# Performance work log

Measured on AMD Instinct MI355X. Metric: run time of the kernel, lower is better.

The kernel has to match this reference:

```python
import jax, jax.numpy as jnp
import numpy as np

MAX_DISPARITY = 48  # disparity range [0, 48] -> 49 hypotheses


def setup_inputs() -> dict:
    key = jax.random.key(0)
    k1, k2, k3, k4 = jax.random.split(key, 4)
    B, C, H, W = 1, 64, 256, 512
    C_out = 16
    return {
        "left_embedding": jax.random.normal(k1, (B, C, H, W), dtype=jnp.float32),
        "right_embedding": jax.random.normal(k2, (B, C, H, W), dtype=jnp.float32),
        "W_op": jax.random.normal(k3, (C_out, 2 * C), dtype=jnp.float32) * 0.05,
        "b_op": jax.random.normal(k4, (C_out,), dtype=jnp.float32) * 0.05,
    }


def reference(left_embedding, right_embedding, W_op, b_op):
    # operation(cat([L, R_shift], dim=1)) with a 1x1 conv is linear, so it
    # splits into W_l @ L + W_r @ R_shift; shifting commutes with the 1x1 conv,
    # so we apply the conv ONCE to each embedding and shift the small result.
    D = MAX_DISPARITY
    B, C, H, W = left_embedding.shape
    W_l, W_r = W_op[:, :C], W_op[:, C:]
    L = jnp.einsum('oc,bcyx->boyx', W_l, left_embedding)    # [B,O,H,W]
    R = jnp.einsum('oc,bcyx->boyx', W_r, right_embedding)   # [B,O,H,W]
    # ZeroPad2d((D, 0, 0, 0)): pad D zeros on the LEFT of the x axis
    R_pad = jnp.pad(R, ((0, 0), (0, 0), (0, 0), (D, 0)))
    # disparity d reads padded[..., D-d : D-d+W] -> idx[d, x] = D - d + x
    idx = (D - jnp.arange(D + 1))[:, None] + jnp.arange(W)[None, :]  # [D+1, W]
    R_shift = R_pad[:, :, :, idx]                  # [B,O,H,D+1,W]
    R_shift = jnp.transpose(R_shift, (0, 1, 3, 2, 4))  # [B,O,D+1,H,W]
    out = L[:, :, None, :, :] + R_shift + b_op[None, :, None, None, None]
    return out  # [batch, feature, disparity, y, x]
```

## Files before the change

kernel.cpp:

```cpp
#include <hip/hip_runtime.h>

#define HH 256
#define WW 512
#define CC 64
#define CO 16
#define DD 48
#define ND (DD + 1)

typedef float f32x4 __attribute__((ext_vector_type(4)));

__global__ __launch_bounds__(256) void lr_project(
    const float* __restrict__ left, const float* __restrict__ right,
    const float* __restrict__ Wop, const float* __restrict__ bop,
    float* __restrict__ Lout, float* __restrict__ Rout)
{
    const int tid = blockIdx.x * blockDim.x + threadIdx.x;
    const int x = tid & (WW - 1);
    const int y = tid >> 9;

    float accL[CO], accR[CO];
#pragma unroll
    for (int o = 0; o < CO; ++o) { accL[o] = 0.0f; accR[o] = 0.0f; }

#pragma unroll 4
    for (int c = 0; c < CC; ++c) {
        const float l = left [(c * HH + y) * WW + x];
        const float r = right[(c * HH + y) * WW + x];
#pragma unroll
        for (int o = 0; o < CO; ++o) {
            accL[o] += Wop[o * (2 * CC) + c]      * l;
            accR[o] += Wop[o * (2 * CC) + CC + c] * r;
        }
    }

#pragma unroll
    for (int o = 0; o < CO; ++o) {
        Lout[(o * HH + y) * WW + x] = accL[o] + bop[o];
        Rout[(o * HH + y) * WW + x] = accR[o];
    }
}

__global__ __launch_bounds__(256) void assemble_plane(
    const float* __restrict__ L, const float* __restrict__ R,
    float* __restrict__ out)
{
    const int g = blockIdx.x & 7;
    const int j = blockIdx.x >> 3;
    const int o = 2 * g + (j / ND);
    const int d = j % ND;
    const int od = o * ND + d;

    const int t  = threadIdx.x;
    const int x4 = t & 127;
    const int y0 = t >> 7;
    const int x  = x4 * 4;

    const float m0 = (x + 0 >= d) ? 1.0f : 0.0f;
    const float m1 = (x + 1 >= d) ? 1.0f : 0.0f;
    const float m2 = (x + 2 >= d) ? 1.0f : 0.0f;
    const float m3 = (x + 3 >= d) ? 1.0f : 0.0f;

    const float* Lp = &L[(o * HH + y0) * WW + x];
    const float* Rp = Lp + (R - L) - d;
    float*       op = &out[((size_t)od * HH + y0) * WW + x];

#pragma unroll 4
    for (int k = 0; k < HH / 2; ++k) {
        const f32x4 lv = *reinterpret_cast<const f32x4*>(Lp);
        f32x4 rv;
        __builtin_memcpy(&rv, Rp, sizeof(rv));

        f32x4 ov;
        ov.x = lv.x + m0 * rv.x;
        ov.y = lv.y + m1 * rv.y;
        ov.z = lv.z + m2 * rv.z;
        ov.w = lv.w + m3 * rv.w;
        __builtin_nontemporal_store(ov, reinterpret_cast<f32x4*>(op));

        Lp += 2 * WW;
        Rp += 2 * WW;
        op += 2 * WW;
    }
}

extern "C" void kernel_launch(void* const* d_in, const int* in_sizes, int n_in,
                              void* d_out, int out_size, void* d_ws, size_t ws_size,
                              hipStream_t stream) {
    const float* left  = (const float*)d_in[0];
    const float* right = (const float*)d_in[1];
    const float* Wop   = (const float*)d_in[2];
    const float* bop   = (const float*)d_in[3];
    float* out = (float*)d_out;

    float* Lws = (float*)d_ws;
    float* Rws = Lws + (size_t)CO * HH * WW;

    lr_project<<<(HH * WW) / 256, 256, 0, stream>>>(left, right, Wop, bop, Lws, Rws);

    assemble_plane<<<CO * ND, 256, 0, stream>>>(Lws, Rws, out);
}
```

Baseline: 123.9 us.

## Replace per-plane assembly with persistent wave-linear streaming over output

The broadcast-add kernel becomes a fixed grid of 1024 waves, each streaming a contiguous 392×1KB span of the output. It splits the span at (feature, disparity) plane boundaries to recompute the shift and masks. Odd half-rows skip the mask multiply, since only x<48 can need masking. Stores switch from nontemporal to normal cached stores. Work is split evenly across waves with long sequential write runs, at the cost of per-segment bookkeeping and possible cache pollution from the regular stores.

```diff
diff --git a/kernel.cpp b/kernel.cpp
--- a/kernel.cpp
+++ b/kernel.cpp
@@ -40,46 +40,58 @@
     }
 }
 
-__global__ __launch_bounds__(256) void assemble_plane(
+__global__ __launch_bounds__(256) void assemble_stream(
     const float* __restrict__ L, const float* __restrict__ R,
     float* __restrict__ out)
 {
-    const int g = blockIdx.x & 7;
-    const int j = blockIdx.x >> 3;
-    const int o = 2 * g + (j / ND);
-    const int d = j % ND;
-    const int od = o * ND + d;
+    const int tid  = blockIdx.x * blockDim.x + threadIdx.x;
+    const int wave = tid >> 6;
+    const int lane = tid & 63;
 
-    const int t  = threadIdx.x;
-    const int x4 = t & 127;
-    const int y0 = t >> 7;
-    const int x  = x4 * 4;
+    int v = wave * 392;
+    const int vend = v + 392;
 
-    const float m0 = (x + 0 >= d) ? 1.0f : 0.0f;
-    const float m1 = (x + 1 >= d) ? 1.0f : 0.0f;
-    const float m2 = (x + 2 >= d) ? 1.0f : 0.0f;
-    const float m3 = (x + 3 >= d) ? 1.0f : 0.0f;
+    float* op = out + (size_t)v * 256 + lane * 4;
+    const ptrdiff_t RminusL = R - L;
 
-    const float* Lp = &L[(o * HH + y0) * WW + x];
-    const float* Rp = Lp + (R - L) - d;
-    float*       op = &out[((size_t)od * HH + y0) * WW + x];
+    while (v < vend) {
+        const int od = v >> 9;
+        const int o  = od / ND;
+        const int d  = od - o * ND;
+        const int segend = min(vend, (od + 1) << 9);
+        int w = v & 511;
+
+        const int xb = lane * 4;
+        const float m0 = (xb + 0 >= d) ? 1.0f : 0.0f;
+        const float m1 = (xb + 1 >= d) ? 1.0f : 0.0f;
+        const float m2 = (xb + 2 >= d) ? 1.0f : 0.0f;
+        const float m3 = (xb + 3 >= d) ? 1.0f : 0.0f;
+
+        const float* lp = L + (size_t)o * (HH * WW) + (size_t)w * 256 + lane * 4;
+        const float* rp = lp + RminusL - d;
 
 #pragma unroll 4
-    for (int k = 0; k < HH / 2; ++k) {
-        const f32x4 lv = *reinterpret_cast<const f32x4*>(Lp);
-        f32x4 rv;
-        __builtin_memcpy(&rv, Rp, sizeof(rv));
+        for (; v < segend; ++v, ++w) {
+            f32x4 lv = *reinterpret_cast<const f32x4*>(lp);
+            f32x4 rv;
+            __builtin_memcpy(&rv, rp, sizeof(rv));
 
-        f32x4 ov;
-        ov.x = lv.x + m0 * rv.x;
-        ov.y = lv.y + m1 * rv.y;
-        ov.z = lv.z + m2 * rv.z;
-        ov.w = lv.w + m3 * rv.w;
-        __builtin_nontemporal_store(ov, reinterpret_cast<f32x4*>(op));
+            f32x4 ov;
+            if (w & 1) {
+                ov.x = lv.x + rv.x;
+                ov.y = lv.y + rv.y;
+                ov.z = lv.z + rv.z;
+                ov.w = lv.w + rv.w;
+            } else {
+                ov.x = lv.x + m0 * rv.x;
+                ov.y = lv.y + m1 * rv.y;
+                ov.z = lv.z + m2 * rv.z;
+                ov.w = lv.w + m3 * rv.w;
+            }
+            *reinterpret_cast<f32x4*>(op) = ov;
 
-        Lp += 2 * WW;
-        Rp += 2 * WW;
-        op += 2 * WW;
+            lp += 256; rp += 256; op += 256;
+        }
     }
 }
 
@@ -97,5 +109,5 @@
 
     lr_project<<<(HH * WW) / 256, 256, 0, stream>>>(left, right, Wop, bop, Lws, Rws);
 
-    assemble_plane<<<CO * ND, 256, 0, stream>>>(Lws, Rws, out);
+    assemble_stream<<<256, 256, 0, stream>>>(Lws, Rws, out);
 }
```

New measurement: 210.6 us. +70.0%, slower.
